# Kernel tuning notes

Hardware: AMD Instinct MI355X
Metric: run time of the kernel (lower is better)

The kernel has to match this reference:

```python
import jax, jax.numpy as jnp
import numpy as np

P, C, D = 65536, 64, 256

def setup_inputs() -> dict:
    key = jax.random.key(0)
    k1, k2, k3, k4 = jax.random.split(key, 4)
    return {
        "protos1": jax.random.normal(k1, (P, D), dtype=jnp.float32),
        "protos2": jax.random.normal(k2, (P, D), dtype=jnp.float32),
        "W": jax.random.normal(k3, (D, D), dtype=jnp.float32) / np.float32(np.sqrt(D)),
        "b": jax.random.normal(k4, (D,), dtype=jnp.float32),
        "num_classes": C,
    }

def _pairwise_dist(x, y):
    # x: (C, n, D), y: (C, m, D) -> squared-euclidean-style dists (C, n, m)
    xs = jnp.sum(x * x, axis=-1)[:, :, None]
    ys = jnp.sum(y * y, axis=-1)[:, None, :]
    return xs + ys - 2.0 * jnp.einsum('cid,cjd->cij', x, y)

def reference(protos1, protos2, W, b, num_classes):
    nc = int(num_classes)
    d = protos1.shape[-1]
    # prototypes[c::num_classes] for all c at once: (P,D) -> (P//C, C, D) -> (C, P//C, D)
    p1 = protos1.reshape(-1, nc, d).transpose(1, 0, 2)
    p2 = protos2.reshape(-1, nc, d).transpose(1, 0, 2)
    # transition: nn.Linear -> x @ W.T + b ; inverse: (x - b) @ inv(W.T)
    p2_inv = (p2 - b) @ jnp.linalg.inv(W.T)
    p1_fwd = p1 @ W.T + b
    a = _pairwise_dist(p1, p2_inv)          # (C, n, n)
    bb = _pairwise_dist(p2, p1_fwd)         # (C, n, n)
    proto_losses_source = jnp.mean(jnp.min(a, axis=2), axis=1)   # (C,)
    proto_losses_target = jnp.mean(jnp.min(bb, axis=2), axis=1)  # (C,)
    return jnp.stack([proto_losses_source, proto_losses_target])  # (2, C)
```

## Files before the change

### kernel.cpp

```cpp
#include <hip/hip_runtime.h>

#define D 256
#define NC 64

using u16 = unsigned short;
using u32 = unsigned int;

typedef __attribute__((ext_vector_type(8))) short bfv8;
typedef __attribute__((ext_vector_type(4))) float f32x4;

__device__ __forceinline__ float bf2f(u32 u) {
  union { u32 i; float f; } v; v.i = u << 16; return v.f;
}
__device__ __forceinline__ u16 f2bf(float f) {
  union { float f; u32 i; } v; v.f = f;
  u32 x = v.i;
  return (u16)((x + 0x7FFFu + ((x >> 16) & 1u)) >> 16);
}
__device__ __forceinline__ u32 pk2(float a, float b) {
  return (u32)f2bf(a) | ((u32)f2bf(b) << 16);
}
__device__ __forceinline__ size_t cmrow(int g) {
  return (size_t)(((g & 63) << 10) | (g >> 6));
}

__device__ __forceinline__ void gload_lds16(const void* src, void* dst) {
  __builtin_amdgcn_global_load_lds(
      (const __attribute__((address_space(1))) void*)src,
      (__attribute__((address_space(3))) void*)dst, 16, 0, 0);
}

#define PH_LDS 70912
#define DIST_LDS 66560

__device__ void gj_body(const float* __restrict__ W, float* __restrict__ IW,
                        char* smem) {
  float (*Ml)[20]    = (float(*)[20])smem;
  float (*Arow)[256] = (float(*)[256])(smem + 20480);
  float (*G)[256]    = (float(*)[256])(smem + 36864);
  u16*  Gfrag        = (u16*)(smem + 53248);
  float (*Pinv)[20]  = (float(*)[20])(smem + 69632);
  const int t = threadIdx.x, w = t >> 6, l = t & 63;
  const int lj = l & 15, lh = l >> 4;
  const int r0 = 32 * w;

  f32x4 x[2][16];
#pragma unroll
  for (int rt = 0; rt < 2; ++rt)
#pragma unroll
    for (int ct = 0; ct < 16; ++ct)
#pragma unroll
      for (int reg = 0; reg < 4; ++reg)
        x[rt][ct][reg] = W[(size_t)(r0 + 16 * rt + 4 * lh + reg) * D + 16 * ct + lj];

  for (int s = 0; s < 16; ++s) {
    const int pw = s >> 1, ph = s & 1;
#pragma unroll
    for (int rt = 0; rt < 2; ++rt)
#pragma unroll
      for (int ct = 0; ct < 16; ++ct)
        if (ct == s)
#pragma unroll
          for (int reg = 0; reg < 4; ++reg)
            Ml[r0 + 16 * rt + 4 * lh + reg][lj] = x[rt][ct][reg];
    if (w == pw) {
#pragma unroll
      for (int rt = 0; rt < 2; ++rt)
        if (rt == ph)
#pragma unroll
          for (int ct = 0; ct < 16; ++ct)
#pragma unroll
            for (int reg = 0; reg < 4; ++reg)
              Arow[4 * lh + reg][16 * ct + lj] = x[rt][ct][reg];
    }
    __syncthreads();
    if (t < 16) {
      float p[16];
      {
        float4 rr0 = *(const float4*)&Ml[16 * s + t][0];
        float4 rr1 = *(const float4*)&Ml[16 * s + t][4];
        float4 rr2 = *(const float4*)&Ml[16 * s + t][8];
        float4 rr3 = *(const float4*)&Ml[16 * s + t][12];
        p[0] = rr0.x; p[1] = rr0.y; p[2] = rr0.z; p[3] = rr0.w;
        p[4] = rr1.x; p[5] = rr1.y; p[6] = rr1.z; p[7] = rr1.w;
        p[8] = rr2.x; p[9] = rr2.y; p[10] = rr2.z; p[11] = rr2.w;
        p[12] = rr3.x; p[13] = rr3.y; p[14] = rr3.z; p[15] = rr3.w;
      }
#pragma unroll
      for (int pp = 0; pp < 16; ++pp) {
        float u[16];
#pragma unroll
        for (int j = 0; j < 16; ++j)
          u[j] = __int_as_float(__builtin_amdgcn_readlane(__float_as_int(p[j]), pp));
        const float pv = u[pp];
        const float d = 1.0f / pv;
        if (t == pp) {
#pragma unroll
          for (int j = 0; j < 16; ++j) p[j] = u[j] * d;
          p[pp] = d;
        } else {
          const float md = p[pp] * d;
          u[pp] = pv + 1.0f;
#pragma unroll
          for (int j = 0; j < 16; ++j) p[j] = fmaf(-md, u[j], p[j]);
        }
      }
#pragma unroll
      for (int j = 0; j < 16; ++j) Pinv[t][j] = p[j];
    }
    __syncthreads();
    {
      const bool inC = ((l >> 2) == s);
      const int co = (l & 3) << 2;
      const int gct = l >> 2;
#pragma unroll
      for (int h = 0; h < 2; ++h) {
        const int kk = 2 * w + h;
        float4 g = make_float4(0.f, 0.f, 0.f, 0.f);
#pragma unroll
        for (int q = 0; q < 16; ++q) {
          const float pv = Pinv[kk][q];
          const float4 av = *(const float4*)&Arow[q][4 * l];
          g.x = fmaf(pv, av.x, g.x); g.y = fmaf(pv, av.y, g.y);
          g.z = fmaf(pv, av.z, g.z); g.w = fmaf(pv, av.w, g.w);
        }
        if (inC) {
          g.x = Pinv[kk][co + 0] + (kk == co + 0 ? 1.f : 0.f);
          g.y = Pinv[kk][co + 1] + (kk == co + 1 ? 1.f : 0.f);
          g.z = Pinv[kk][co + 2] + (kk == co + 2 ? 1.f : 0.f);
          g.w = Pinv[kk][co + 3] + (kk == co + 3 ? 1.f : 0.f);
        }
        *(float4*)&G[kk][4 * l] = g;
        const int e0 = kk & 7;
        const int lbase = 16 * (kk >> 3);
        const float gv[4] = {g.x, g.y, g.z, g.w};
#pragma unroll
        for (int cc = 0; cc < 4; ++cc) {
          const int cl = 4 * (l & 3) + cc;
          const u16 hi = f2bf(gv[cc]);
          const u16 lo = f2bf(gv[cc] - bf2f(hi));
          Gfrag[(gct * 64 + lbase + cl) * 8 + e0] = hi;
          Gfrag[(gct * 64 + 32 + lbase + cl) * 8 + e0] = lo;
        }
      }
    }
    __syncthreads();
    bfv8 afr[2];
#pragma unroll
    for (int rt = 0; rt < 2; ++rt) {
      const int row = r0 + 16 * rt + lj;
      float4 f0 = *(const float4*)&Ml[row][8 * (lh & 1)];
      float4 f1 = *(const float4*)&Ml[row][8 * (lh & 1) + 4];
      const float fv[8] = {f0.x, f0.y, f0.z, f0.w, f1.x, f1.y, f1.z, f1.w};
      union { bfv8 v; u16 e[8]; } A;
      if (lh < 2) {
#pragma unroll
        for (int e = 0; e < 8; ++e) A.e[e] = f2bf(-fv[e]);
      } else {
#pragma unroll
        for (int e = 0; e < 8; ++e) {
          const float hi = bf2f(f2bf(fv[e]));
          A.e[e] = f2bf(-(fv[e] - hi));
        }
      }
      afr[rt] = A.v;
    }
#pragma unroll
    for (int rt = 0; rt < 2; ++rt) {
      const bool skip = (w == pw) && (rt == ph);
      if (!skip) {
#pragma unroll
        for (int ct = 0; ct < 16; ++ct) {
          bfv8 b1 = *(const bfv8*)&Gfrag[(ct * 64 + l) * 8];
          bfv8 b2 = *(const bfv8*)&Gfrag[(ct * 64 + (l ^ 32)) * 8];
          x[rt][ct] = __builtin_amdgcn_mfma_f32_16x16x32_bf16(afr[rt], b1, x[rt][ct], 0, 0, 0);
          x[rt][ct] = __builtin_amdgcn_mfma_f32_16x16x32_bf16(afr[rt], b2, x[rt][ct], 0, 0, 0);
        }
      }
    }
    if (w == pw) {
#pragma unroll
      for (int rt = 0; rt < 2; ++rt)
        if (rt == ph)
#pragma unroll
          for (int ct = 0; ct < 16; ++ct) {
            if (ct == s) {
#pragma unroll
              for (int reg = 0; reg < 4; ++reg)
                x[rt][ct][reg] = Pinv[4 * lh + reg][lj];
            } else {
#pragma unroll
              for (int reg = 0; reg < 4; ++reg)
                x[rt][ct][reg] = G[4 * lh + reg][16 * ct + lj];
            }
          }
    }
    __syncthreads();
  }
#pragma unroll
  for (int rt = 0; rt < 2; ++rt)
#pragma unroll
    for (int ct = 0; ct < 16; ++ct)
#pragma unroll
      for (int reg = 0; reg < 4; ++reg)
        IW[(size_t)(r0 + 16 * rt + 4 * lh + reg) * D + 16 * ct + lj] = x[rt][ct][reg];
}

template <int MODE, bool WRITE_NRM>
__device__ void prep_body(const float* __restrict__ Ain,
                          const u16* __restrict__ Brows,
                          const float* __restrict__ biasv,
                          u16* __restrict__ Out, float* __restrict__ nrm,
                          float* __restrict__ nfp, int bid, char* smem) {
  const int it = bid >> 1, jh = bid & 1;
  const int tx = threadIdx.x, ww = tx >> 6, l = tx & 63;
  const int mw = ww >> 2, nw = ww & 3, l4 = l >> 4, lm = l & 15;
  char* Ab = smem;
  float* nfpart = (float*)(smem + 65536);

  bfv8 bfr[2][8];
#pragma unroll
  for (int nf = 0; nf < 2; ++nf)
#pragma unroll
    for (int ks = 0; ks < 8; ++ks)
      bfr[nf][ks] = *(const bfv8*)(Brows +
          (size_t)(jh * 128 + nw * 32 + nf * 16 + lm) * D + ks * 32 + l4 * 8);

  {
    const int r = tx >> 2, q = tx & 3;
    const float* arow = Ain + (size_t)(it * 128 + r) * D;
    float ss = 0.f;
#pragma unroll
    for (int kk = 0; kk < 2; ++kk) {
      const int ks = q * 2 + kk;
#pragma unroll
      for (int g2 = 0; g2 < 4; ++g2) {
        float4 v0 = *(const float4*)(arow + ks * 32 + g2 * 8);
        float4 v1 = *(const float4*)(arow + ks * 32 + g2 * 8 + 4);
        ss = fmaf(v0.x, v0.x, fmaf(v0.y, v0.y, fmaf(v0.z, v0.z, fmaf(v0.w, v0.w, ss))));
        ss = fmaf(v1.x, v1.x, fmaf(v1.y, v1.y, fmaf(v1.z, v1.z, fmaf(v1.w, v1.w, ss))));
        uint4 w4;
        w4.x = pk2(v0.x, v0.y); w4.y = pk2(v0.z, v0.w);
        w4.z = pk2(v1.x, v1.y); w4.w = pk2(v1.z, v1.w);
        *(uint4*)(Ab + ((ks * 8 + (r >> 4)) * 64 + g2 * 16 + (r & 15)) * 16) = w4;
      }
    }
    ss += __shfl_xor(ss, 1, 64);
    ss += __shfl_xor(ss, 2, 64);
    if (WRITE_NRM && q == 0) nrm[cmrow(it * 128 + r)] = ss;
  }
  __syncthreads();

  const bfv8* A8 = (const bfv8*)Ab;
  f32x4 acc[4][2];
#pragma unroll
  for (int mf = 0; mf < 4; ++mf) {
    acc[mf][0] = f32x4{0.f, 0.f, 0.f, 0.f};
    acc[mf][1] = f32x4{0.f, 0.f, 0.f, 0.f};
  }
#pragma unroll
  for (int ks = 0; ks < 8; ++ks)
#pragma unroll
    for (int mf = 0; mf < 4; ++mf) {
      bfv8 a = A8[(ks * 8 + mw * 4 + mf) * 64 + l];
      acc[mf][0] = __builtin_amdgcn_mfma_f32_16x16x32_bf16(a, bfr[0][ks], acc[mf][0], 0, 0, 0);
      acc[mf][1] = __builtin_amdgcn_mfma_f32_16x16x32_bf16(a, bfr[1][ks], acc[mf][1], 0, 0, 0);
    }

  float bias[2];
  if (MODE == 0) {
#pragma unroll
    for (int nf = 0; nf < 2; ++nf)
      bias[nf] = biasv[jh * 128 + nw * 32 + nf * 16 + lm];
  } else {
#pragma unroll
    for (int nf = 0; nf < 2; ++nf) {
      float pd = 0.f;
#pragma unroll
      for (int ks = 0; ks < 8; ++ks) {
        float4 b0 = *(const float4*)(biasv + ks * 32 + l4 * 8);
        float4 b1 = *(const float4*)(biasv + ks * 32 + l4 * 8 + 4);
        pd = fmaf(b0.x, bf2f((u16)bfr[nf][ks][0]), pd);
        pd = fmaf(b0.y, bf2f((u16)bfr[nf][ks][1]), pd);
        pd = fmaf(b0.z, bf2f((u16)bfr[nf][ks][2]), pd);
        pd = fmaf(b0.w, bf2f((u16)bfr[nf][ks][3]), pd);
        pd = fmaf(b1.x, bf2f((u16)bfr[nf][ks][4]), pd);
        pd = fmaf(b1.y, bf2f((u16)bfr[nf][ks][5]), pd);
        pd = fmaf(b1.z, bf2f((u16)bfr[nf][ks][6]), pd);
        pd = fmaf(b1.w, bf2f((u16)bfr[nf][ks][7]), pd);
      }
      pd += __shfl_xor(pd, 16, 64);
      pd += __shfl_xor(pd, 32, 64);
      bias[nf] = -pd;
    }
  }

#pragma unroll
  for (int mf = 0; mf < 4; ++mf)
#pragma unroll
    for (int rr = 0; rr < 4; ++rr) {
      const int g = it * 128 + mw * 64 + mf * 16 + l4 * 4 + rr;
      const size_t orow = cmrow(g) * D;
      float v2 = 0.f;
#pragma unroll
      for (int nf = 0; nf < 2; ++nf) {
        const float v = acc[mf][nf][rr] + bias[nf];
        const u16 hv = f2bf(v);
        Out[orow + jh * 128 + nw * 32 + nf * 16 + lm] = hv;
        const float vr = bf2f(hv);
        v2 = fmaf(vr, vr, v2);
      }
      v2 += __shfl_xor(v2, 1, 64);
      v2 += __shfl_xor(v2, 2, 64);
      v2 += __shfl_xor(v2, 4, 64);
      v2 += __shfl_xor(v2, 8, 64);
      if (lm == 0) nfpart[nw * 128 + mw * 64 + mf * 16 + l4 * 4 + rr] = v2;
    }
  __syncthreads();
  if (tx < 128) {
    float s = nfpart[tx] + nfpart[128 + tx] + nfpart[256 + tx] + nfpart[384 + tx];
    nfp[cmrow(it * 128 + tx)] = s;
  }
}

__device__ void norms_role(const float* __restrict__ p2, float* __restrict__ n2,
                           int idx) {
  const int tx = threadIdx.x, q = tx & 3;
#pragma unroll
  for (int rep = 0; rep < 8; ++rep) {
    const int g = idx * 1024 + rep * 128 + (tx >> 2);
    const float* row = p2 + (size_t)g * D + q * 64;
    float ss = 0.f;
#pragma unroll
    for (int g2 = 0; g2 < 16; ++g2) {
      float4 v = *(const float4*)(row + g2 * 4);
      ss = fmaf(v.x, v.x, fmaf(v.y, v.y, fmaf(v.z, v.z, fmaf(v.w, v.w, ss))));
    }
    ss += __shfl_xor(ss, 1, 64);
    ss += __shfl_xor(ss, 2, 64);
    if (q == 0) n2[cmrow(g)] = ss;
  }
}

__global__ __launch_bounds__(512) void phase1_kernel(
    const float* __restrict__ p1, const float* __restrict__ p2,
    const float* __restrict__ W, const u16* __restrict__ Wb,
    const float* __restrict__ bv, u16* __restrict__ Fb,
    float* __restrict__ n1, float* __restrict__ n2,
    float* __restrict__ nfp0, float* __restrict__ nfp1,
    float* __restrict__ IWa) {
  extern __shared__ char smem[];
  const int b = blockIdx.x;
  if (b == 0) {
    gj_body(W, IWa, smem);
  } else if (b <= 1024) {
    const int bid = b - 1;
    prep_body<0, true>(p1, Wb, bv, Fb, n1, (bid & 1) ? nfp1 : nfp0, bid, smem);
  } else {
    norms_role(p2, n2, b - 1025);
  }
}

__global__ __launch_bounds__(512, 4) void phase3_kernel(
    const float* __restrict__ p2, const u16* __restrict__ IWb,
    const float* __restrict__ bv, u16* __restrict__ Qb,
    float* __restrict__ nqp0, float* __restrict__ nqp1) {
  extern __shared__ char smem[];
  const int bid = blockIdx.x;
  prep_body<1, false>(p2, IWb, bv, Qb, nullptr,
                      (bid & 1) ? nqp1 : nqp0, bid, smem);
}

__global__ __launch_bounds__(256) void nr_residual(const float* __restrict__ W,
                                                   const float* __restrict__ X,
                                                   float* __restrict__ R) {
  __shared__ float wrow[D];
  const int i = blockIdx.x, j = threadIdx.x;
  wrow[j] = W[i * D + j];
  __syncthreads();
  float acc = 0.f;
#pragma unroll 8
  for (int k = 0; k < D; ++k) acc = fmaf(wrow[k], X[k * D + j], acc);
  R[i * D + j] = (i == j ? 2.0f : 0.0f) - acc;
}

__global__ __launch_bounds__(256) void nr_mult_bf16(const float* __restrict__ X,
                                                    const float* __restrict__ R,
                                                    u16* __restrict__ Yb) {
  __shared__ float xrow[D];
  const int i = blockIdx.x, j = threadIdx.x;
  xrow[j] = X[i * D + j];
  __syncthreads();
  float acc = 0.f;
#pragma unroll 8
  for (int k = 0; k < D; ++k) acc = fmaf(xrow[k], R[k * D + j], acc);
  Yb[i * D + j] = f2bf(acc);
}

__global__ __launch_bounds__(256) void wconv(const float* __restrict__ W,
                                             u16* __restrict__ Wb) {
  const int i = blockIdx.x * 256 + threadIdx.x;
  Wb[i] = f2bf(W[i]);
}

__global__ __launch_bounds__(256, 2) void dist_kernel(
    const float* __restrict__ p1, const float* __restrict__ p2,
    const u16* __restrict__ Qb, const u16* __restrict__ Fb,
    const float* __restrict__ n1, const float* __restrict__ n2,
    const float* __restrict__ nqp0, const float* __restrict__ nqp1,
    const float* __restrict__ nfp0, const float* __restrict__ nfp1,
    float* __restrict__ partial) {
  extern __shared__ char smem[];
  const int bid = blockIdx.x;
  const int lb = (bid & 7) * 128 + (bid >> 3);
  const int c = lb >> 4, dir = (lb >> 3) & 1, it = lb & 7;
  const float* Ain = dir ? p2 : p1;
  const u16* Bin = dir ? Fb : Qb;
  const float* nA = dir ? n2 : n1;
  const float* nB0 = dir ? nfp0 : nqp0;
  const float* nB1 = dir ? nfp1 : nqp1;
  const int tx = threadIdx.x, wid = tx >> 6, l = tx & 63;
  const int l4 = l >> 4, lm = l & 15;

  auto issue_b = [&](int half, int jt) {
    const size_t base = ((size_t)(c << 10) + jt * 128) * D;
#pragma unroll
    for (int jf = 0; jf < 8; ++jf) {
      const u16* src = Bin + base + (size_t)(jf * 16 + lm) * D
                       + half * 128 + wid * 32 + l4 * 8;
      gload_lds16(src, smem + half * 32768 + (wid * 8 + jf) * 1024);
    }
  };

  issue_b(0, 0);
  bfv8 afr[2][8];
  const float* abase = Ain + ((size_t)(it * 128 + wid * 32) * NC + c) * D;
#pragma unroll
  for (int m = 0; m < 2; ++m)
#pragma unroll
    for (int ks = 0; ks < 8; ++ks) {
      const float* ap = abase + (size_t)(m * 16 + lm) * (NC * D) + ks * 32 + l4 * 8;
      float4 v0 = *(const float4*)(ap);
      float4 v1 = *(const float4*)(ap + 4);
      union { bfv8 v; uint4 u; } cv;
      cv.u.x = pk2(v0.x, v0.y); cv.u.y = pk2(v0.z, v0.w);
      cv.u.z = pk2(v1.x, v1.y); cv.u.w = pk2(v1.z, v1.w);
      afr[m][ks] = cv.v;
    }
  float na[2][4];
#pragma unroll
  for (int m = 0; m < 2; ++m)
#pragma unroll
    for (int rr = 0; rr < 4; ++rr)
      na[m][rr] = nA[(c << 10) + it * 128 + wid * 32 + m * 16 + l4 * 4 + rr];
  float minv[2][4];
#pragma unroll
  for (int m = 0; m < 2; ++m)
#pragma unroll
    for (int rr = 0; rr < 4; ++rr) minv[m][rr] = 3.0e38f;
  __syncthreads();

  const bfv8* lds8 = (const bfv8*)smem;
  for (int jt = 0; jt < 8; ++jt) {
    f32x4 acc[2][8];
#pragma unroll
    for (int m = 0; m < 2; ++m)
#pragma unroll
      for (int n = 0; n < 8; ++n) acc[m][n] = f32x4{0.f, 0.f, 0.f, 0.f};
    float nbv[8];
#pragma unroll
    for (int n = 0; n < 8; ++n) {
      const int idx = (c << 10) + jt * 128 + n * 16 + lm;
      nbv[n] = nB0[idx] + nB1[idx];
    }
    issue_b(1, jt);
#pragma unroll
    for (int ks = 0; ks < 4; ++ks) {
      bfv8 bb[8];
#pragma unroll
      for (int n = 0; n < 8; ++n) bb[n] = lds8[(ks * 8 + n) * 64 + l];
#pragma unroll
      for (int m = 0; m < 2; ++m)
#pragma unroll
        for (int n = 0; n < 8; ++n)
          acc[m][n] = __builtin_amdgcn_mfma_f32_16x16x32_bf16(afr[m][ks], bb[n], acc[m][n], 0, 0, 0);
    }
    __syncthreads();
    if (jt < 7) issue_b(0, jt + 1);
#pragma unroll
    for (int ks = 4; ks < 8; ++ks) {
      bfv8 bb[8];
#pragma unroll
      for (int n = 0; n < 8; ++n) bb[n] = lds8[2048 + ((ks - 4) * 8 + n) * 64 + l];
#pragma unroll
      for (int m = 0; m < 2; ++m)
#pragma unroll
        for (int n = 0; n < 8; ++n)
          acc[m][n] = __builtin_amdgcn_mfma_f32_16x16x32_bf16(afr[m][ks], bb[n], acc[m][n], 0, 0, 0);
    }
#pragma unroll
    for (int m = 0; m < 2; ++m)
#pragma unroll
      for (int n = 0; n < 8; ++n)
#pragma unroll
        for (int rr = 0; rr < 4; ++rr) {
          const float dd = na[m][rr] + nbv[n] - 2.0f * acc[m][n][rr];
          minv[m][rr] = fminf(minv[m][rr], dd);
        }
    __syncthreads();
  }
  float* red = (float*)(smem + 65536);
#pragma unroll
  for (int m = 0; m < 2; ++m)
#pragma unroll
    for (int rr = 0; rr < 4; ++rr) {
      float mm = minv[m][rr];
      mm = fminf(mm, __shfl_xor(mm, 1, 64));
      mm = fminf(mm, __shfl_xor(mm, 2, 64));
      mm = fminf(mm, __shfl_xor(mm, 4, 64));
      mm = fminf(mm, __shfl_xor(mm, 8, 64));
      if (lm == 0) red[wid * 32 + m * 16 + l4 * 4 + rr] = mm;
    }
  __syncthreads();
  if (tx < 128) {
    float v = red[tx];
#pragma unroll
    for (int off = 32; off; off >>= 1) v += __shfl_xor(v, off, 64);
    if ((tx & 63) == 0) red[128 + (tx >> 6)] = v;
  }
  __syncthreads();
  if (tx == 0) partial[lb] = red[128] + red[129];
}

__global__ void finalize_kernel(const float* __restrict__ partial,
                                float* __restrict__ out) {
  const int tx = threadIdx.x;
  if (tx >= 128) return;
  const int dir = tx >> 6, c = tx & 63;
  float s = 0.f;
#pragma unroll
  for (int it = 0; it < 8; ++it) s += partial[(c << 4) | (dir << 3) | it];
  out[dir * 64 + c] = s * (1.0f / 1024.0f);
}

extern "C" void kernel_launch(void* const* d_in, const int* in_sizes, int n_in,
                              void* d_out, int out_size, void* d_ws, size_t ws_size,
                              hipStream_t stream) {
  const float* p1 = (const float*)d_in[0];
  const float* p2 = (const float*)d_in[1];
  const float* W  = (const float*)d_in[2];
  const float* bv = (const float*)d_in[3];
  float* out = (float*)d_out;
  char* ws = (char*)d_ws;
  float* n1   = (float*)(ws);
  float* n2   = (float*)(ws + (256 << 10));
  float* nfp0 = (float*)(ws + (512 << 10));
  float* nfp1 = (float*)(ws + (768 << 10));
  float* nqp0 = (float*)(ws + (1024 << 10));
  float* nqp1 = (float*)(ws + (1280 << 10));
  float* partial = (float*)(ws + (1536 << 10));
  u16* Wb  = (u16*)(ws + (1544 << 10));
  u16* IWb = (u16*)(ws + (1672 << 10));
  float* IWa = (float*)(ws + (1800 << 10));
  float* Rt  = (float*)(ws + (2056 << 10));
  u16* Fb  = (u16*)(ws + (2560 << 10));
  u16* Qb  = (u16*)(ws + (2560 << 10) + (32u << 20));

  hipFuncSetAttribute((const void*)phase1_kernel,
                      hipFuncAttributeMaxDynamicSharedMemorySize, PH_LDS);
  hipFuncSetAttribute((const void*)phase3_kernel,
                      hipFuncAttributeMaxDynamicSharedMemorySize, PH_LDS);
  hipFuncSetAttribute((const void*)dist_kernel,
                      hipFuncAttributeMaxDynamicSharedMemorySize, DIST_LDS);

  wconv<<<256, 256, 0, stream>>>(W, Wb);
  phase1_kernel<<<1089, 512, PH_LDS, stream>>>(p1, p2, W, Wb, bv, Fb,
                                               n1, n2, nfp0, nfp1, IWa);
  nr_residual<<<256, 256, 0, stream>>>(W, IWa, Rt);
  nr_mult_bf16<<<256, 256, 0, stream>>>(IWa, Rt, IWb);
  phase3_kernel<<<1024, 512, PH_LDS, stream>>>(p2, IWb, bv, Qb, nqp0, nqp1);
  dist_kernel<<<1024, 256, DIST_LDS, stream>>>(p1, p2, Qb, Fb, n1, n2,
                                               nqp0, nqp1, nfp0, nfp1, partial);
  finalize_kernel<<<1, 128, 0, stream>>>(partial, out);
}
```

Measured before the change: 339.5 us.

## Use 1024-thread blocks so each prep block computes all output columns

The prep kernels (forward W projection and inverse projection) now run 1024-thread blocks with 16 waves laid out as 2x8. Each block covers all 256 output columns of its 128 rows, so the A tile is converted to bf16 once rather than twice per column half, and the norm partials are written once. That removes the split nfp0/nfp1 and nqp0/nqp1 buffers and the extra add in the distance kernel. The Gauss-Jordan inverse body is restructured to 16 waves with one 16-row strip each. The cost is launch_bounds(1024,1), which allows one block per CU with a tighter register budget, and fewer blocks overall.

```diff
diff --git a/kernel.cpp b/kernel.cpp
--- a/kernel.cpp
+++ b/kernel.cpp
@@ -42,36 +42,28 @@
   float (*Pinv)[20]  = (float(*)[20])(smem + 69632);
   const int t = threadIdx.x, w = t >> 6, l = t & 63;
   const int lj = l & 15, lh = l >> 4;
-  const int r0 = 32 * w;
-
-  f32x4 x[2][16];
-#pragma unroll
-  for (int rt = 0; rt < 2; ++rt)
+  const int r0 = 16 * w;
+
+  f32x4 x[16];
+#pragma unroll
+  for (int ct = 0; ct < 16; ++ct)
+#pragma unroll
+    for (int reg = 0; reg < 4; ++reg)
+      x[ct][reg] = W[(size_t)(r0 + 4 * lh + reg) * D + 16 * ct + lj];
+
+  for (int s = 0; s < 16; ++s) {
 #pragma unroll
     for (int ct = 0; ct < 16; ++ct)
-#pragma unroll
-      for (int reg = 0; reg < 4; ++reg)
-        x[rt][ct][reg] = W[(size_t)(r0 + 16 * rt + 4 * lh + reg) * D + 16 * ct + lj];
-
-  for (int s = 0; s < 16; ++s) {
-    const int pw = s >> 1, ph = s & 1;
-#pragma unroll
-    for (int rt = 0; rt < 2; ++rt)
+      if (ct == s)
+#pragma unroll
+        for (int reg = 0; reg < 4; ++reg)
+          Ml[r0 + 4 * lh + reg][lj] = x[ct][reg];
+    if (w == s) {
 #pragma unroll
       for (int ct = 0; ct < 16; ++ct)
-        if (ct == s)
-#pragma unroll
-          for (int reg = 0; reg < 4; ++reg)
-            Ml[r0 + 16 * rt + 4 * lh + reg][lj] = x[rt][ct][reg];
-    if (w == pw) {
-#pragma unroll
-      for (int rt = 0; rt < 2; ++rt)
-        if (rt == ph)
-#pragma unroll
-          for (int ct = 0; ct < 16; ++ct)
-#pragma unroll
-            for (int reg = 0; reg < 4; ++reg)
-              Arow[4 * lh + reg][16 * ct + lj] = x[rt][ct][reg];
+#pragma unroll
+        for (int reg = 0; reg < 4; ++reg)
+          Arow[4 * lh + reg][16 * ct + lj] = x[ct][reg];
     }
     __syncthreads();
     if (t < 16) {
@@ -113,42 +105,38 @@
       const bool inC = ((l >> 2) == s);
       const int co = (l & 3) << 2;
       const int gct = l >> 2;
-#pragma unroll
-      for (int h = 0; h < 2; ++h) {
-        const int kk = 2 * w + h;
-        float4 g = make_float4(0.f, 0.f, 0.f, 0.f);
-#pragma unroll
-        for (int q = 0; q < 16; ++q) {
-          const float pv = Pinv[kk][q];
-          const float4 av = *(const float4*)&Arow[q][4 * l];
-          g.x = fmaf(pv, av.x, g.x); g.y = fmaf(pv, av.y, g.y);
-          g.z = fmaf(pv, av.z, g.z); g.w = fmaf(pv, av.w, g.w);
-        }
-        if (inC) {
-          g.x = Pinv[kk][co + 0] + (kk == co + 0 ? 1.f : 0.f);
-          g.y = Pinv[kk][co + 1] + (kk == co + 1 ? 1.f : 0.f);
-          g.z = Pinv[kk][co + 2] + (kk == co + 2 ? 1.f : 0.f);
-          g.w = Pinv[kk][co + 3] + (kk == co + 3 ? 1.f : 0.f);
-        }
-        *(float4*)&G[kk][4 * l] = g;
-        const int e0 = kk & 7;
-        const int lbase = 16 * (kk >> 3);
-        const float gv[4] = {g.x, g.y, g.z, g.w};
-#pragma unroll
-        for (int cc = 0; cc < 4; ++cc) {
-          const int cl = 4 * (l & 3) + cc;
-          const u16 hi = f2bf(gv[cc]);
-          const u16 lo = f2bf(gv[cc] - bf2f(hi));
-          Gfrag[(gct * 64 + lbase + cl) * 8 + e0] = hi;
-          Gfrag[(gct * 64 + 32 + lbase + cl) * 8 + e0] = lo;
-        }
+      const int kk = w;
+      float4 g = make_float4(0.f, 0.f, 0.f, 0.f);
+#pragma unroll
+      for (int q = 0; q < 16; ++q) {
+        const float pv = Pinv[kk][q];
+        const float4 av = *(const float4*)&Arow[q][4 * l];
+        g.x = fmaf(pv, av.x, g.x); g.y = fmaf(pv, av.y, g.y);
+        g.z = fmaf(pv, av.z, g.z); g.w = fmaf(pv, av.w, g.w);
+      }
+      if (inC) {
+        g.x = Pinv[kk][co + 0] + (kk == co + 0 ? 1.f : 0.f);
+        g.y = Pinv[kk][co + 1] + (kk == co + 1 ? 1.f : 0.f);
+        g.z = Pinv[kk][co + 2] + (kk == co + 2 ? 1.f : 0.f);
+        g.w = Pinv[kk][co + 3] + (kk == co + 3 ? 1.f : 0.f);
+      }
+      *(float4*)&G[kk][4 * l] = g;
+      const int e0 = kk & 7;
+      const int lbase = 16 * (kk >> 3);
+      const float gv[4] = {g.x, g.y, g.z, g.w};
+#pragma unroll
+      for (int cc = 0; cc < 4; ++cc) {
+        const int cl = 4 * (l & 3) + cc;
+        const u16 hi = f2bf(gv[cc]);
+        const u16 lo = f2bf(gv[cc] - bf2f(hi));
+        Gfrag[(gct * 64 + lbase + cl) * 8 + e0] = hi;
+        Gfrag[(gct * 64 + 32 + lbase + cl) * 8 + e0] = lo;
       }
     }
     __syncthreads();
-    bfv8 afr[2];
-#pragma unroll
-    for (int rt = 0; rt < 2; ++rt) {
-      const int row = r0 + 16 * rt + lj;
+    bfv8 afr;
+    {
+      const int row = r0 + lj;
       float4 f0 = *(const float4*)&Ml[row][8 * (lh & 1)];
       float4 f1 = *(const float4*)&Ml[row][8 * (lh & 1) + 4];
       const float fv[8] = {f0.x, f0.y, f0.z, f0.w, f1.x, f1.y, f1.z, f1.w};
@@ -163,47 +151,37 @@
           A.e[e] = f2bf(-(fv[e] - hi));
         }
       }
-      afr[rt] = A.v;
-    }
-#pragma unroll
-    for (int rt = 0; rt < 2; ++rt) {
-      const bool skip = (w == pw) && (rt == ph);
-      if (!skip) {
-#pragma unroll
-        for (int ct = 0; ct < 16; ++ct) {
-          bfv8 b1 = *(const bfv8*)&Gfrag[(ct * 64 + l) * 8];
-          bfv8 b2 = *(const bfv8*)&Gfrag[(ct * 64 + (l ^ 32)) * 8];
-          x[rt][ct] = __builtin_amdgcn_mfma_f32_16x16x32_bf16(afr[rt], b1, x[rt][ct], 0, 0, 0);
-          x[rt][ct] = __builtin_amdgcn_mfma_f32_16x16x32_bf16(afr[rt], b2, x[rt][ct], 0, 0, 0);
+      afr = A.v;
+    }
+    if (w != s) {
+#pragma unroll
+      for (int ct = 0; ct < 16; ++ct) {
+        bfv8 b1 = *(const bfv8*)&Gfrag[(ct * 64 + l) * 8];
+        bfv8 b2 = *(const bfv8*)&Gfrag[(ct * 64 + (l ^ 32)) * 8];
+        x[ct] = __builtin_amdgcn_mfma_f32_16x16x32_bf16(afr, b1, x[ct], 0, 0, 0);
+        x[ct] = __builtin_amdgcn_mfma_f32_16x16x32_bf16(afr, b2, x[ct], 0, 0, 0);
+      }
+    } else {
+#pragma unroll
+      for (int ct = 0; ct < 16; ++ct) {
+        if (ct == s) {
+#pragma unroll
+          for (int reg = 0; reg < 4; ++reg)
+            x[ct][reg] = Pinv[4 * lh + reg][lj];
+        } else {
+#pragma unroll
+          for (int reg = 0; reg < 4; ++reg)
+            x[ct][reg] = G[4 * lh + reg][16 * ct + lj];
         }
       }
     }
-    if (w == pw) {
-#pragma unroll
-      for (int rt = 0; rt < 2; ++rt)
-        if (rt == ph)
-#pragma unroll
-          for (int ct = 0; ct < 16; ++ct) {
-            if (ct == s) {
-#pragma unroll
-              for (int reg = 0; reg < 4; ++reg)
-                x[rt][ct][reg] = Pinv[4 * lh + reg][lj];
-            } else {
-#pragma unroll
-              for (int reg = 0; reg < 4; ++reg)
-                x[rt][ct][reg] = G[4 * lh + reg][16 * ct + lj];
-            }
-          }
-    }
     __syncthreads();
   }
 #pragma unroll
-  for (int rt = 0; rt < 2; ++rt)
-#pragma unroll
-    for (int ct = 0; ct < 16; ++ct)
-#pragma unroll
-      for (int reg = 0; reg < 4; ++reg)
-        IW[(size_t)(r0 + 16 * rt + 4 * lh + reg) * D + 16 * ct + lj] = x[rt][ct][reg];
+  for (int ct = 0; ct < 16; ++ct)
+#pragma unroll
+    for (int reg = 0; reg < 4; ++reg)
+      IW[(size_t)(r0 + 4 * lh + reg) * D + 16 * ct + lj] = x[ct][reg];
 }
 
 template <int MODE, bool WRITE_NRM>
@@ -211,43 +189,39 @@
                           const u16* __restrict__ Brows,
                           const float* __restrict__ biasv,
                           u16* __restrict__ Out, float* __restrict__ nrm,
-                          float* __restrict__ nfp, int bid, char* smem) {
-  const int it = bid >> 1, jh = bid & 1;
+                          float* __restrict__ nfp, int it, char* smem) {
   const int tx = threadIdx.x, ww = tx >> 6, l = tx & 63;
-  const int mw = ww >> 2, nw = ww & 3, l4 = l >> 4, lm = l & 15;
+  const int mw = ww >> 3, nw = ww & 7, l4 = l >> 4, lm = l & 15;
   char* Ab = smem;
   float* nfpart = (float*)(smem + 65536);
 
   bfv8 bfr[2][8];
 #pragma unroll
-  for (int nf = 0; nf < 2; ++nf)
+  for (int nf2 = 0; nf2 < 2; ++nf2)
 #pragma unroll
     for (int ks = 0; ks < 8; ++ks)
-      bfr[nf][ks] = *(const bfv8*)(Brows +
-          (size_t)(jh * 128 + nw * 32 + nf * 16 + lm) * D + ks * 32 + l4 * 8);
+      bfr[nf2][ks] = *(const bfv8*)(Brows +
+          (size_t)(nw * 32 + nf2 * 16 + lm) * D + ks * 32 + l4 * 8);
 
   {
-    const int r = tx >> 2, q = tx & 3;
-    const float* arow = Ain + (size_t)(it * 128 + r) * D;
+    const int r = tx >> 3, sg = tx & 7;
+    const float* arow = Ain + (size_t)(it * 128 + r) * D + sg * 32;
     float ss = 0.f;
 #pragma unroll
-    for (int kk = 0; kk < 2; ++kk) {
-      const int ks = q * 2 + kk;
-#pragma unroll
-      for (int g2 = 0; g2 < 4; ++g2) {
-        float4 v0 = *(const float4*)(arow + ks * 32 + g2 * 8);
-        float4 v1 = *(const float4*)(arow + ks * 32 + g2 * 8 + 4);
-        ss = fmaf(v0.x, v0.x, fmaf(v0.y, v0.y, fmaf(v0.z, v0.z, fmaf(v0.w, v0.w, ss))));
-        ss = fmaf(v1.x, v1.x, fmaf(v1.y, v1.y, fmaf(v1.z, v1.z, fmaf(v1.w, v1.w, ss))));
-        uint4 w4;
-        w4.x = pk2(v0.x, v0.y); w4.y = pk2(v0.z, v0.w);
-        w4.z = pk2(v1.x, v1.y); w4.w = pk2(v1.z, v1.w);
-        *(uint4*)(Ab + ((ks * 8 + (r >> 4)) * 64 + g2 * 16 + (r & 15)) * 16) = w4;
-      }
+    for (int g2 = 0; g2 < 4; ++g2) {
+      float4 v0 = *(const float4*)(arow + g2 * 8);
+      float4 v1 = *(const float4*)(arow + g2 * 8 + 4);
+      ss = fmaf(v0.x, v0.x, fmaf(v0.y, v0.y, fmaf(v0.z, v0.z, fmaf(v0.w, v0.w, ss))));
+      ss = fmaf(v1.x, v1.x, fmaf(v1.y, v1.y, fmaf(v1.z, v1.z, fmaf(v1.w, v1.w, ss))));
+      uint4 w4;
+      w4.x = pk2(v0.x, v0.y); w4.y = pk2(v0.z, v0.w);
+      w4.z = pk2(v1.x, v1.y); w4.w = pk2(v1.z, v1.w);
+      *(uint4*)(Ab + (sg * 8 + (r >> 4)) * 1024 + ((r & 15) + g2 * 16) * 16) = w4;
     }
     ss += __shfl_xor(ss, 1, 64);
     ss += __shfl_xor(ss, 2, 64);
-    if (WRITE_NRM && q == 0) nrm[cmrow(it * 128 + r)] = ss;
+    ss += __shfl_xor(ss, 4, 64);
+    if (WRITE_NRM && sg == 0) nrm[cmrow(it * 128 + r)] = ss;
   }
   __syncthreads();
 
@@ -270,28 +244,28 @@
   float bias[2];
   if (MODE == 0) {
 #pragma unroll
-    for (int nf = 0; nf < 2; ++nf)
-      bias[nf] = biasv[jh * 128 + nw * 32 + nf * 16 + lm];
+    for (int nf2 = 0; nf2 < 2; ++nf2)
+      bias[nf2] = biasv[nw * 32 + nf2 * 16 + lm];
   } else {
 #pragma unroll
-    for (int nf = 0; nf < 2; ++nf) {
+    for (int nf2 = 0; nf2 < 2; ++nf2) {
       float pd = 0.f;
 #pragma unroll
       for (int ks = 0; ks < 8; ++ks) {
         float4 b0 = *(const float4*)(biasv + ks * 32 + l4 * 8);
         float4 b1 = *(const float4*)(biasv + ks * 32 + l4 * 8 + 4);
-        pd = fmaf(b0.x, bf2f((u16)bfr[nf][ks][0]), pd);
-        pd = fmaf(b0.y, bf2f((u16)bfr[nf][ks][1]), pd);
-        pd = fmaf(b0.z, bf2f((u16)bfr[nf][ks][2]), pd);
-        pd = fmaf(b0.w, bf2f((u16)bfr[nf][ks][3]), pd);
-        pd = fmaf(b1.x, bf2f((u16)bfr[nf][ks][4]), pd);
-        pd = fmaf(b1.y, bf2f((u16)bfr[nf][ks][5]), pd);
-        pd = fmaf(b1.z, bf2f((u16)bfr[nf][ks][6]), pd);
-        pd = fmaf(b1.w, bf2f((u16)bfr[nf][ks][7]), pd);
+        pd = fmaf(b0.x, bf2f((u16)bfr[nf2][ks][0]), pd);
+        pd = fmaf(b0.y, bf2f((u16)bfr[nf2][ks][1]), pd);
+        pd = fmaf(b0.z, bf2f((u16)bfr[nf2][ks][2]), pd);
+        pd = fmaf(b0.w, bf2f((u16)bfr[nf2][ks][3]), pd);
+        pd = fmaf(b1.x, bf2f((u16)bfr[nf2][ks][4]), pd);
+        pd = fmaf(b1.y, bf2f((u16)bfr[nf2][ks][5]), pd);
+        pd = fmaf(b1.z, bf2f((u16)bfr[nf2][ks][6]), pd);
+        pd = fmaf(b1.w, bf2f((u16)bfr[nf2][ks][7]), pd);
       }
       pd += __shfl_xor(pd, 16, 64);
       pd += __shfl_xor(pd, 32, 64);
-      bias[nf] = -pd;
+      bias[nf2] = -pd;
     }
   }
 
@@ -303,10 +277,10 @@
       const size_t orow = cmrow(g) * D;
       float v2 = 0.f;
 #pragma unroll
-      for (int nf = 0; nf < 2; ++nf) {
-        const float v = acc[mf][nf][rr] + bias[nf];
+      for (int nf2 = 0; nf2 < 2; ++nf2) {
+        const float v = acc[mf][nf2][rr] + bias[nf2];
         const u16 hv = f2bf(v);
-        Out[orow + jh * 128 + nw * 32 + nf * 16 + lm] = hv;
+        Out[orow + nw * 32 + nf2 * 16 + lm] = hv;
         const float vr = bf2f(hv);
         v2 = fmaf(vr, vr, v2);
       }
@@ -318,7 +292,9 @@
     }
   __syncthreads();
   if (tx < 128) {
-    float s = nfpart[tx] + nfpart[128 + tx] + nfpart[256 + tx] + nfpart[384 + tx];
+    float s = 0.f;
+#pragma unroll
+    for (int q = 0; q < 8; ++q) s += nfpart[q * 128 + tx];
     nfp[cmrow(it * 128 + tx)] = s;
   }
 }
@@ -328,7 +304,7 @@
   const int tx = threadIdx.x, q = tx & 3;
 #pragma unroll
   for (int rep = 0; rep < 8; ++rep) {
-    const int g = idx * 1024 + rep * 128 + (tx >> 2);
+    const int g = idx * 2048 + rep * 256 + (tx >> 2);
     const float* row = p2 + (size_t)g * D + q * 64;
     float ss = 0.f;
 #pragma unroll
@@ -342,33 +318,29 @@
   }
 }
 
-__global__ __launch_bounds__(512) void phase1_kernel(
+__global__ __launch_bounds__(1024, 1) void phase1_kernel(
     const float* __restrict__ p1, const float* __restrict__ p2,
     const float* __restrict__ W, const u16* __restrict__ Wb,
     const float* __restrict__ bv, u16* __restrict__ Fb,
     float* __restrict__ n1, float* __restrict__ n2,
-    float* __restrict__ nfp0, float* __restrict__ nfp1,
-    float* __restrict__ IWa) {
+    float* __restrict__ nf, float* __restrict__ IWa) {
   extern __shared__ char smem[];
   const int b = blockIdx.x;
   if (b == 0) {
     gj_body(W, IWa, smem);
-  } else if (b <= 1024) {
-    const int bid = b - 1;
-    prep_body<0, true>(p1, Wb, bv, Fb, n1, (bid & 1) ? nfp1 : nfp0, bid, smem);
+  } else if (b <= 512) {
+    prep_body<0, true>(p1, Wb, bv, Fb, n1, nf, b - 1, smem);
   } else {
-    norms_role(p2, n2, b - 1025);
-  }
-}
-
-__global__ __launch_bounds__(512, 4) void phase3_kernel(
+    norms_role(p2, n2, b - 513);
+  }
+}
+
+__global__ __launch_bounds__(1024, 1) void phase3_kernel(
     const float* __restrict__ p2, const u16* __restrict__ IWb,
     const float* __restrict__ bv, u16* __restrict__ Qb,
-    float* __restrict__ nqp0, float* __restrict__ nqp1) {
+    float* __restrict__ nq) {
   extern __shared__ char smem[];
-  const int bid = blockIdx.x;
-  prep_body<1, false>(p2, IWb, bv, Qb, nullptr,
-                      (bid & 1) ? nqp1 : nqp0, bid, smem);
+  prep_body<1, false>(p2, IWb, bv, Qb, nullptr, nq, blockIdx.x, smem);
 }
 
 __global__ __launch_bounds__(256) void nr_residual(const float* __restrict__ W,
@@ -407,8 +379,7 @@
     const float* __restrict__ p1, const float* __restrict__ p2,
     const u16* __restrict__ Qb, const u16* __restrict__ Fb,
     const float* __restrict__ n1, const float* __restrict__ n2,
-    const float* __restrict__ nqp0, const float* __restrict__ nqp1,
-    const float* __restrict__ nfp0, const float* __restrict__ nfp1,
+    const float* __restrict__ nq, const float* __restrict__ nf,
     float* __restrict__ partial) {
   extern __shared__ char smem[];
   const int bid = blockIdx.x;
@@ -417,8 +388,7 @@
   const float* Ain = dir ? p2 : p1;
   const u16* Bin = dir ? Fb : Qb;
   const float* nA = dir ? n2 : n1;
-  const float* nB0 = dir ? nfp0 : nqp0;
-  const float* nB1 = dir ? nfp1 : nqp1;
+  const float* nB = dir ? nf : nq;
   const int tx = threadIdx.x, wid = tx >> 6, l = tx & 63;
   const int l4 = l >> 4, lm = l & 15;
 
@@ -469,10 +439,8 @@
       for (int n = 0; n < 8; ++n) acc[m][n] = f32x4{0.f, 0.f, 0.f, 0.f};
     float nbv[8];
 #pragma unroll
-    for (int n = 0; n < 8; ++n) {
-      const int idx = (c << 10) + jt * 128 + n * 16 + lm;
-      nbv[n] = nB0[idx] + nB1[idx];
-    }
+    for (int n = 0; n < 8; ++n)
+      nbv[n] = nB[(c << 10) + jt * 128 + n * 16 + lm];
     issue_b(1, jt);
 #pragma unroll
     for (int ks = 0; ks < 4; ++ks) {
@@ -554,17 +522,15 @@
   char* ws = (char*)d_ws;
   float* n1   = (float*)(ws);
   float* n2   = (float*)(ws + (256 << 10));
-  float* nfp0 = (float*)(ws + (512 << 10));
-  float* nfp1 = (float*)(ws + (768 << 10));
-  float* nqp0 = (float*)(ws + (1024 << 10));
-  float* nqp1 = (float*)(ws + (1280 << 10));
-  float* partial = (float*)(ws + (1536 << 10));
-  u16* Wb  = (u16*)(ws + (1544 << 10));
-  u16* IWb = (u16*)(ws + (1672 << 10));
-  float* IWa = (float*)(ws + (1800 << 10));
-  float* Rt  = (float*)(ws + (2056 << 10));
-  u16* Fb  = (u16*)(ws + (2560 << 10));
-  u16* Qb  = (u16*)(ws + (2560 << 10) + (32u << 20));
+  float* nf   = (float*)(ws + (512 << 10));
+  float* nq   = (float*)(ws + (768 << 10));
+  float* partial = (float*)(ws + (1024 << 10));
+  u16* Wb  = (u16*)(ws + (1032 << 10));
+  u16* IWb = (u16*)(ws + (1160 << 10));
+  float* IWa = (float*)(ws + (1288 << 10));
+  float* Rt  = (float*)(ws + (1544 << 10));
+  u16* Fb  = (u16*)(ws + (2048 << 10));
+  u16* Qb  = (u16*)(ws + (2048 << 10) + (32u << 20));
 
   hipFuncSetAttribute((const void*)phase1_kernel,
                       hipFuncAttributeMaxDynamicSharedMemorySize, PH_LDS);
@@ -574,12 +540,12 @@
                       hipFuncAttributeMaxDynamicSharedMemorySize, DIST_LDS);
 
   wconv<<<256, 256, 0, stream>>>(W, Wb);
-  phase1_kernel<<<1089, 512, PH_LDS, stream>>>(p1, p2, W, Wb, bv, Fb,
-                                               n1, n2, nfp0, nfp1, IWa);
+  phase1_kernel<<<545, 1024, PH_LDS, stream>>>(p1, p2, W, Wb, bv, Fb,
+                                               n1, n2, nf, IWa);
   nr_residual<<<256, 256, 0, stream>>>(W, IWa, Rt);
   nr_mult_bf16<<<256, 256, 0, stream>>>(IWa, Rt, IWb);
-  phase3_kernel<<<1024, 512, PH_LDS, stream>>>(p2, IWb, bv, Qb, nqp0, nqp1);
+  phase3_kernel<<<512, 1024, PH_LDS, stream>>>(p2, IWb, bv, Qb, nq);
   dist_kernel<<<1024, 256, DIST_LDS, stream>>>(p1, p2, Qb, Fb, n1, n2,
-                                               nqp0, nqp1, nfp0, nfp1, partial);
+                                               nq, nf, partial);
   finalize_kernel<<<1, 128, 0, stream>>>(partial, out);
 }
```

After: 298.1 us. 1.14x faster.
